# Kernel tuning notes

Hardware: AMD Instinct MI355X
Metric: run time of the kernel (lower is better)

## Reference

```python
import jax, jax.numpy as jnp
import numpy as np

N_HEADS = 16
ROPE_BASE = 10000.0


def _rotate_half(x):
    d = x.shape[-1] // 2
    return jnp.concatenate([-x[..., d:], x[..., :d]], axis=-1)


def _rope_tables(L, head_dim, dtype):
    inv_freq = 1.0 / (ROPE_BASE ** (jnp.arange(0, head_dim, 2, dtype=jnp.float32) / head_dim))
    t = jnp.arange(L, dtype=jnp.float32)
    freqs = jnp.outer(t, inv_freq)  # [L, head_dim//2]
    # torch code repeats cos/sin along last dim (tile x2) -> concat([c, c])
    cos = jnp.concatenate([jnp.cos(freqs), jnp.cos(freqs)], axis=-1).astype(dtype)
    sin = jnp.concatenate([jnp.sin(freqs), jnp.sin(freqs)], axis=-1).astype(dtype)
    return cos[None, None], sin[None, None]  # [1,1,L,head_dim]


def setup_inputs() -> dict:
    key = jax.random.key(0)
    kx, kq, kk, kv, ko = jax.random.split(key, 5)
    B, L, D = 4, 2048, 1024
    s = 0.02
    return {
        "x": jax.random.normal(kx, (B, L, D), dtype=jnp.float32),
        "Wq": jax.random.normal(kq, (D, D), dtype=jnp.float32) * s,
        "Wk": jax.random.normal(kk, (D, D), dtype=jnp.float32) * s,
        "Wv": jax.random.normal(kv, (D, D), dtype=jnp.float32) * s,
        "Wo": jax.random.normal(ko, (D, D), dtype=jnp.float32) * s,
    }


def reference(x, Wq, Wk, Wv, Wo):
    B, L, D = x.shape
    H = N_HEADS
    hd = D // H

    def split_heads(y):
        return y.reshape(B, L, H, hd).transpose(0, 2, 1, 3)  # [B,H,L,hd]

    q = split_heads(x @ Wq.T)
    k = split_heads(x @ Wk.T)
    v = split_heads(x @ Wv.T)

    cos, sin = _rope_tables(L, hd, x.dtype)
    q = q * cos + _rotate_half(q) * sin
    k = k * cos + _rotate_half(k) * sin

    scale = 1.0 / jnp.sqrt(jnp.asarray(hd, dtype=x.dtype))
    scores = jnp.einsum("bhqd,bhkd->bhqk", q, k) * scale
    attn = jax.nn.softmax(scores, axis=-1)
    out = jnp.einsum("bhqk,bhkd->bhqd", attn, v)
    out = out.transpose(0, 2, 1, 3).reshape(B, L, D)
    return out @ Wo.T
```

## Files before the change

kernel.cpp:

```cpp
#include <hip/hip_runtime.h>


typedef __bf16 bf16_t;
typedef __bf16 bf16x8 __attribute__((ext_vector_type(8)));
typedef __bf16 bf16x4 __attribute__((ext_vector_type(4)));
typedef float  floatx4 __attribute__((ext_vector_type(4)));
typedef unsigned int u32x2 __attribute__((ext_vector_type(2)));

#define B_  4
#define L_  2048
#define D_  1024
#define H_  16
#define HD_ 64
#define M_  (B_*L_)

__device__ __forceinline__ void async_copy16(const bf16_t* g, bf16_t* l) {
  __builtin_amdgcn_global_load_lds(
      (const __attribute__((address_space(1))) void*)g,
      (__attribute__((address_space(3))) void*)l, 16, 0, 0);
}

__device__ __forceinline__ unsigned int pack_bf16(float a, float b) {
  unsigned short ua = __builtin_bit_cast(unsigned short, (bf16_t)a);
  unsigned short ub = __builtin_bit_cast(unsigned short, (bf16_t)b);
  return (unsigned int)ua | ((unsigned int)ub << 16);
}

__global__ void prep_kernel(const float* __restrict__ x,
                            const float* __restrict__ wq, const float* __restrict__ wk,
                            const float* __restrict__ wv, const float* __restrict__ wo,
                            bf16_t* __restrict__ xb,
                            bf16_t* __restrict__ wqb, bf16_t* __restrict__ wkb,
                            bf16_t* __restrict__ wvb, bf16_t* __restrict__ wob,
                            float* __restrict__ cosT, float* __restrict__ sinT)
{
  const int NX = M_*D_;
  const int NW = D_*D_;
  int i = blockIdx.x*256 + threadIdx.x;
  if (i < NX) { xb[i] = (bf16_t)x[i]; return; }
  i -= NX;
  if (i < NW) { wqb[i] = (bf16_t)wq[i]; return; }
  i -= NW;
  if (i < NW) { wkb[i] = (bf16_t)wk[i]; return; }
  i -= NW;
  if (i < NW) { wvb[i] = (bf16_t)wv[i]; return; }
  i -= NW;
  if (i < NW) { wob[i] = (bf16_t)wo[i]; return; }
  i -= NW;
  if (i < L_*32) {
    int l = i >> 5, f = i & 31;
    double inv = pow(10000.0, -(double)f / 32.0);
    double ang = (double)l * inv;
    cosT[i] = (float)cos(ang);
    sinT[i] = (float)sin(ang);
  }
}

template<int MODE>
__global__ __launch_bounds__(256) void gemm_kernel(
    const bf16_t* __restrict__ A,
    const bf16_t* __restrict__ W0, const bf16_t* __restrict__ W1, const bf16_t* __restrict__ W2,
    bf16_t* __restrict__ C0, bf16_t* __restrict__ C1, bf16_t* __restrict__ C2,
    float* __restrict__ Cf,
    const float* __restrict__ cosT, const float* __restrict__ sinT)
{
  __shared__ __align__(16) bf16_t As[128*64];
  __shared__ __align__(16) bf16_t Bs[128*64];
  const int KD = 1024, ND = 1024;
  int z = (MODE==0) ? (int)blockIdx.z : 0;
  const bf16_t* W = (MODE==1) ? W0 : (z==0 ? W0 : (z==1 ? W1 : W2));
  int m0 = blockIdx.y*128, n0 = blockIdx.x*128;
  int tid = threadIdx.x;
  int wave = tid>>6, lane = tid&63, quad = lane>>4, lr = lane&15;
  int wm = wave>>1, wn = wave&1;
  int srow = lane>>3, sslot = lane&7;

  floatx4 zero4 = {0.f,0.f,0.f,0.f};
  floatx4 acc[4][4];
  #pragma unroll
  for (int i=0;i<4;i++)
    #pragma unroll
    for (int j=0;j<4;j++) acc[i][j] = zero4;

  #pragma unroll 1
  for (int k0 = 0; k0 < KD; k0 += 64) {
    #pragma unroll
    for (int j=0;j<4;j++) {
      int chunk = wave + j*4;
      int row = chunk*8 + srow;
      int col = ((sslot ^ (row&7)) << 3);
      async_copy16(A + (size_t)(m0+row)*KD + k0 + col, &As[chunk*512]);
      async_copy16(W + (size_t)(n0+row)*KD + k0 + col, &Bs[chunk*512]);
    }
    __syncthreads();
    #pragma unroll
    for (int ks=0; ks<2; ks++) {
      bf16x8 af[4], bfr[4];
      #pragma unroll
      for (int mi=0;mi<4;mi++)
        af[mi] = *(const bf16x8*)&As[(wm*64+mi*16+lr)*64 + (((ks*4+quad) ^ (lr&7))<<3)];
      #pragma unroll
      for (int ni=0;ni<4;ni++)
        bfr[ni] = *(const bf16x8*)&Bs[(wn*64+ni*16+lr)*64 + (((ks*4+quad) ^ (lr&7))<<3)];
      #pragma unroll
      for (int mi=0;mi<4;mi++)
        #pragma unroll
        for (int ni=0;ni<4;ni++)
          acc[mi][ni] = __builtin_amdgcn_mfma_f32_16x16x32_bf16(af[mi], bfr[ni], acc[mi][ni], 0,0,0);
    }
    __syncthreads();
  }

  if (MODE==1) {
    #pragma unroll
    for (int mi=0;mi<4;mi++) {
      int row = m0 + wm*64 + mi*16 + quad*4;
      #pragma unroll
      for (int ni=0;ni<4;ni++) {
        int col = n0 + wn*64 + ni*16 + lr;
        #pragma unroll
        for (int r=0;r<4;r++)
          Cf[(size_t)(row+r)*ND + col] = acc[mi][ni][r];
      }
    }
  } else if (z < 2) {
    bf16_t* Cb = (z==0) ? C0 : C1;
    const float sc = (z==0) ? 0.18033688011112042f : 1.0f;
    #pragma unroll
    for (int mi=0;mi<4;mi++) {
      int row = m0 + wm*64 + mi*16 + quad*4;
      int l = row & 2047;
      #pragma unroll
      for (int ni=0;ni<2;ni++) {
        int col = n0 + wn*64 + ni*16 + lr;
        int f = ni*16 + lr;
        #pragma unroll
        for (int r=0;r<4;r++) {
          float c = cosT[(l+r)*32 + f];
          float s = sinT[(l+r)*32 + f];
          float lo = acc[mi][ni][r], hi = acc[mi][ni+2][r];
          Cb[(size_t)(row+r)*ND + col]      = (bf16_t)((lo*c - hi*s)*sc);
          Cb[(size_t)(row+r)*ND + col + 32] = (bf16_t)((hi*c + lo*s)*sc);
        }
      }
    }
  } else {
    #pragma unroll
    for (int mi=0;mi<4;mi++) {
      int row0 = m0 + wm*64 + mi*16 + quad*4;
      int bb = row0 >> 11, ll = row0 & 2047;
      #pragma unroll
      for (int ni=0;ni<4;ni++) {
        int col = n0 + wn*64 + ni*16 + lr;
        int hh = col >> 6, dd = col & 63;
        uint2 val;
        val.x = pack_bf16(acc[mi][ni][0], acc[mi][ni][1]);
        val.y = pack_bf16(acc[mi][ni][2], acc[mi][ni][3]);
        *(uint2*)&C2[((size_t)((bb<<4)+hh)*64 + dd)*2048 + ll] = val;
      }
    }
  }
}

__global__ __launch_bounds__(256) void attn_kernel(
    const bf16_t* __restrict__ Q, const bf16_t* __restrict__ K,
    const bf16_t* __restrict__ Vt, bf16_t* __restrict__ Op,
    float* __restrict__ Ls)
{
  __shared__ __align__(16) bf16_t Ks[3][2048];
  __shared__ __align__(16) bf16_t Vs[3][2048];
  int tid = threadIdx.x;
  int wave = tid>>6, lane = tid&63, quad = lane>>4, lr = lane&15;
  int bh = blockIdx.x; int b = bh>>4, h = bh&15;
  int z = blockIdx.z;
  int q0 = blockIdx.y*128 + wave*32;
  size_t rowQ = (size_t)b*L_ + q0;
  int kvbase = z*1024;

  int slr = (lr&3) | ((lr&4)<<1) | ((lr&8)>>1);
  int vg  = ((lr>>2) ^ lr) & 3;

  int ksrow = wave*8 + (lane>>3);
  int kscol = (((lane&7) ^ (ksrow&7)) << 3);
  int vrow  = tid>>2;
  int vscol = (((lane&3) ^ (((vrow>>2)^vrow)&3)) << 3);

  bf16x8 qf[2][2];
  #pragma unroll
  for (int n=0;n<2;n++)
    #pragma unroll
    for (int ks=0;ks<2;ks++)
      qf[n][ks] = *(const bf16x8*)&Q[(rowQ + n*16 + lr)*D_ + h*HD_ + ks*32 + quad*8];

  const bf16_t* Kg = K + ((size_t)b*L_ + kvbase)*D_ + h*HD_;
  const bf16_t* Vg = Vt + ((size_t)bh*HD_)*L_ + kvbase;

  bf16x8 onesf;
  #pragma unroll
  for (int j=0;j<8;j++) onesf[j] = (bf16_t)1.0f;

  floatx4 zero4 = {0.f,0.f,0.f,0.f};
  floatx4 accO[2][4];
  floatx4 accS[2];
  accS[0] = zero4; accS[1] = zero4;
  #pragma unroll
  for (int n=0;n<2;n++)
    #pragma unroll
    for (int dt=0;dt<4;dt++) accO[n][dt] = zero4;

  auto stage = [&](int it, int c) {
    async_copy16(Kg + (size_t)(it*32 + ksrow)*D_ + kscol, &Ks[c][wave*512]);
    async_copy16(Vg + (size_t)vrow*L_ + it*32 + vscol,    &Vs[c][wave*512]);
  };

  stage(0, 0);
  stage(1, 1);
  asm volatile("s_waitcnt vmcnt(2)" ::: "memory");
  __builtin_amdgcn_s_barrier();

  #pragma unroll 1
  for (int it = 0; it < 32; ++it) {
    int c = it % 3;
    if (it < 30) stage(it+2, (it+2) % 3);

    floatx4 St[2][2];
    St[0][0]=zero4; St[0][1]=zero4; St[1][0]=zero4; St[1][1]=zero4;
    __builtin_amdgcn_s_setprio(1);
    #pragma unroll
    for (int t=0;t<2;t++) {
      #pragma unroll
      for (int ks=0;ks<2;ks++) {
        bf16x8 kf = *(const bf16x8*)&Ks[c][(t*16+slr)*64 + (((ks*4+quad) ^ (slr&7))<<3)];
        St[0][t] = __builtin_amdgcn_mfma_f32_16x16x32_bf16(kf, qf[0][ks], St[0][t], 0,0,0);
        St[1][t] = __builtin_amdgcn_mfma_f32_16x16x32_bf16(kf, qf[1][ks], St[1][t], 0,0,0);
      }
    }
    __builtin_amdgcn_s_setprio(0);

    bf16x8 pfv[2];
    #pragma unroll
    for (int n=0;n<2;n++) {
      unsigned int w00 = pack_bf16(exp2f(St[n][0][0]), exp2f(St[n][0][1]));
      unsigned int w01 = pack_bf16(exp2f(St[n][0][2]), exp2f(St[n][0][3]));
      unsigned int w10 = pack_bf16(exp2f(St[n][1][0]), exp2f(St[n][1][1]));
      unsigned int w11 = pack_bf16(exp2f(St[n][1][2]), exp2f(St[n][1][3]));
      u32x2 r0 = __builtin_amdgcn_permlane32_swap(w00, w10, false, false);
      u32x2 r1 = __builtin_amdgcn_permlane32_swap(w01, w11, false, false);
      union { unsigned int u[4]; bf16x8 v; } pu;
      pu.u[0] = r0.x; pu.u[1] = r1.x; pu.u[2] = r0.y; pu.u[3] = r1.y;
      pfv[n] = pu.v;
    }

    __builtin_amdgcn_s_setprio(1);
    #pragma unroll
    for (int dt=0;dt<4;dt++) {
      bf16x8 vf = *(const bf16x8*)&Vs[c][(dt*16+lr)*32 + ((quad ^ vg)<<3)];
      accO[0][dt] = __builtin_amdgcn_mfma_f32_16x16x32_bf16(vf, pfv[0], accO[0][dt], 0,0,0);
      accO[1][dt] = __builtin_amdgcn_mfma_f32_16x16x32_bf16(vf, pfv[1], accO[1][dt], 0,0,0);
    }
    accS[0] = __builtin_amdgcn_mfma_f32_16x16x32_bf16(onesf, pfv[0], accS[0], 0,0,0);
    accS[1] = __builtin_amdgcn_mfma_f32_16x16x32_bf16(onesf, pfv[1], accS[1], 0,0,0);
    __builtin_amdgcn_s_setprio(0);

    if (it < 30) {
      asm volatile("s_waitcnt vmcnt(2)" ::: "memory");
    } else {
      asm volatile("s_waitcnt vmcnt(0)" ::: "memory");
    }
    __builtin_amdgcn_s_barrier();
  }

  bf16_t* Opz = Op + (size_t)z*M_*D_;
  #pragma unroll
  for (int n=0;n<2;n++) {
    #pragma unroll
    for (int dt=0;dt<4;dt++) {
      uint2 w;
      w.x = pack_bf16(accO[n][dt][0], accO[n][dt][1]);
      w.y = pack_bf16(accO[n][dt][2], accO[n][dt][3]);
      *(uint2*)&Opz[(rowQ + n*16 + lr)*D_ + h*HD_ + dt*16 + quad*4] = w;
    }
  }
  if (quad == 0) {
    Ls[z*131072 + bh*2048 + q0 + lr]      = accS[0][0];
    Ls[z*131072 + bh*2048 + q0 + 16 + lr] = accS[1][0];
  }
}

__global__ void reduce_kernel(const bf16_t* __restrict__ Op, const float* __restrict__ Ls,
                              bf16_t* __restrict__ O)
{
  int i = blockIdx.x*256 + threadIdx.x;
  size_t e = (size_t)i*4;
  int d  = (int)(e & 1023);
  int bl = (int)(e >> 10);
  int bq = bl >> 11, l = bl & 2047, h = d >> 6;
  int li = (bq*16 + h)*2048 + l;
  float inv = 1.0f / (Ls[li] + Ls[li + 131072]);
  bf16x4 v0 = *(const bf16x4*)&Op[e];
  bf16x4 v1 = *(const bf16x4*)&Op[(size_t)M_*D_ + e];
  bf16x4 r;
  #pragma unroll
  for (int j=0;j<4;j++)
    r[j] = (bf16_t)(((float)v0[j] + (float)v1[j]) * inv);
  *(bf16x4*)&O[e] = r;
}

extern "C" void kernel_launch(void* const* d_in, const int* in_sizes, int n_in,
                              void* d_out, int out_size, void* d_ws, size_t ws_size,
                              hipStream_t stream) {
  const float* x  = (const float*)d_in[0];
  const float* wq = (const float*)d_in[1];
  const float* wk = (const float*)d_in[2];
  const float* wv = (const float*)d_in[3];
  const float* wo = (const float*)d_in[4];

  char* ws = (char*)d_ws;
  bf16_t* xb  = (bf16_t*)(ws);
  bf16_t* Qb  = (bf16_t*)(ws + (size_t)(16u<<20));
  bf16_t* Kb  = (bf16_t*)(ws + (size_t)(32u<<20));
  bf16_t* Vtb = (bf16_t*)(ws + (size_t)(48u<<20));
  bf16_t* wqb = (bf16_t*)(ws + (size_t)(64u<<20));
  bf16_t* wkb = (bf16_t*)(ws + (size_t)(66u<<20));
  bf16_t* wvb = (bf16_t*)(ws + (size_t)(68u<<20));
  bf16_t* wob = (bf16_t*)(ws + (size_t)(70u<<20));
  float* cosT = (float*)(ws + (size_t)(72u<<20));
  float* sinT = (float*)(ws + (size_t)(72u<<20) + (256u<<10));
  float* Ls   = (float*)wqb;
  bf16_t* Opart = (bf16_t*)d_out;
  bf16_t* Ob = xb;

  prep_kernel<<<49408, 256, 0, stream>>>(x, wq, wk, wv, wo, xb, wqb, wkb, wvb, wob, cosT, sinT);
  gemm_kernel<0><<<dim3(8,64,3), 256, 0, stream>>>(xb, wqb, wkb, wvb, Qb, Kb, Vtb, nullptr, cosT, sinT);
  attn_kernel<<<dim3(64,16,2), 256, 0, stream>>>(Qb, Kb, Vtb, Opart, Ls);
  reduce_kernel<<<8192, 256, 0, stream>>>(Opart, Ls, Ob);
  gemm_kernel<1><<<dim3(8,64,1), 256, 0, stream>>>(Ob, wob, nullptr, nullptr,
                                                   nullptr, nullptr, nullptr, (float*)d_out, cosT, sinT);
}
```

Measured before the change: 330.3 us.

## Drop split-KV attention and reduce kernel; use 64-key tiles with in-kernel normalization

Attention no longer splits the key range in two across blockIdx.z with a separate reduce kernel. Each block now walks the full key range with 64-key tiles in doubled LDS buffers and normalizes the output by the row sum before writing it. This removes the partial-output writes, the reduce launch and its memory traffic. In exchange there are half as many attention blocks (1024 instead of 2048) and more LDS per block, which can lower occupancy and latency hiding. The s_setprio hints are also dropped.

Result: no change. 326.2 us (-1.3%).

```diff
diff --git a/kernel.cpp b/kernel.cpp
--- a/kernel.cpp
+++ b/kernel.cpp
@@ -164,26 +164,20 @@
 
 __global__ __launch_bounds__(256) void attn_kernel(
     const bf16_t* __restrict__ Q, const bf16_t* __restrict__ K,
-    const bf16_t* __restrict__ Vt, bf16_t* __restrict__ Op,
-    float* __restrict__ Ls)
+    const bf16_t* __restrict__ Vt, bf16_t* __restrict__ O)
 {
-  __shared__ __align__(16) bf16_t Ks[3][2048];
-  __shared__ __align__(16) bf16_t Vs[3][2048];
+  __shared__ __align__(16) bf16_t Ks[3][4096];
+  __shared__ __align__(16) bf16_t Vs[3][4096];
   int tid = threadIdx.x;
   int wave = tid>>6, lane = tid&63, quad = lane>>4, lr = lane&15;
   int bh = blockIdx.x; int b = bh>>4, h = bh&15;
-  int z = blockIdx.z;
   int q0 = blockIdx.y*128 + wave*32;
   size_t rowQ = (size_t)b*L_ + q0;
-  int kvbase = z*1024;
 
   int slr = (lr&3) | ((lr&4)<<1) | ((lr&8)>>1);
-  int vg  = ((lr>>2) ^ lr) & 3;
-
-  int ksrow = wave*8 + (lane>>3);
-  int kscol = (((lane&7) ^ (ksrow&7)) << 3);
-  int vrow  = tid>>2;
-  int vscol = (((lane&3) ^ (((vrow>>2)^vrow)&3)) << 3);
+
+  int srow8 = lane>>3;
+  int sslot = lane&7;
 
   bf16x8 qf[2][2];
   #pragma unroll
@@ -192,8 +186,8 @@
     for (int ks=0;ks<2;ks++)
       qf[n][ks] = *(const bf16x8*)&Q[(rowQ + n*16 + lr)*D_ + h*HD_ + ks*32 + quad*8];
 
-  const bf16_t* Kg = K + ((size_t)b*L_ + kvbase)*D_ + h*HD_;
-  const bf16_t* Vg = Vt + ((size_t)bh*HD_)*L_ + kvbase;
+  const bf16_t* Kg = K + (size_t)b*L_*D_ + h*HD_;
+  const bf16_t* Vg = Vt + (size_t)bh*HD_*L_;
 
   bf16x8 onesf;
   #pragma unroll
@@ -209,13 +203,18 @@
     for (int dt=0;dt<4;dt++) accO[n][dt] = zero4;
 
   auto stage = [&](int it, int c) {
-    async_copy16(Kg + (size_t)(it*32 + ksrow)*D_ + kscol, &Ks[c][wave*512]);
-    async_copy16(Vg + (size_t)vrow*L_ + it*32 + vscol,    &Vs[c][wave*512]);
+    #pragma unroll
+    for (int j=0;j<2;j++) {
+      int row = wave*16 + j*8 + srow8;
+      int col = ((sslot ^ (row&7)) << 3);
+      async_copy16(Kg + (size_t)(it*64 + row)*D_ + col, &Ks[c][(wave*16 + j*8)*64]);
+      async_copy16(Vg + (size_t)row*L_ + it*64 + col,   &Vs[c][(wave*16 + j*8)*64]);
+    }
   };
 
   stage(0, 0);
   stage(1, 1);
-  asm volatile("s_waitcnt vmcnt(2)" ::: "memory");
+  asm volatile("s_waitcnt vmcnt(4)" ::: "memory");
   __builtin_amdgcn_s_barrier();
 
   #pragma unroll 1
@@ -223,11 +222,11 @@
     int c = it % 3;
     if (it < 30) stage(it+2, (it+2) % 3);
 
-    floatx4 St[2][2];
-    St[0][0]=zero4; St[0][1]=zero4; St[1][0]=zero4; St[1][1]=zero4;
-    __builtin_amdgcn_s_setprio(1);
-    #pragma unroll
-    for (int t=0;t<2;t++) {
+    floatx4 St[2][4];
+    #pragma unroll
+    for (int t=0;t<4;t++) { St[0][t]=zero4; St[1][t]=zero4; }
+    #pragma unroll
+    for (int t=0;t<4;t++) {
       #pragma unroll
       for (int ks=0;ks<2;ks++) {
         bf16x8 kf = *(const bf16x8*)&Ks[c][(t*16+slr)*64 + (((ks*4+quad) ^ (slr&7))<<3)];
@@ -235,75 +234,59 @@
         St[1][t] = __builtin_amdgcn_mfma_f32_16x16x32_bf16(kf, qf[1][ks], St[1][t], 0,0,0);
       }
     }
-    __builtin_amdgcn_s_setprio(0);
-
-    bf16x8 pfv[2];
+
+    bf16x8 pfv[2][2];
     #pragma unroll
     for (int n=0;n<2;n++) {
-      unsigned int w00 = pack_bf16(exp2f(St[n][0][0]), exp2f(St[n][0][1]));
-      unsigned int w01 = pack_bf16(exp2f(St[n][0][2]), exp2f(St[n][0][3]));
-      unsigned int w10 = pack_bf16(exp2f(St[n][1][0]), exp2f(St[n][1][1]));
-      unsigned int w11 = pack_bf16(exp2f(St[n][1][2]), exp2f(St[n][1][3]));
-      u32x2 r0 = __builtin_amdgcn_permlane32_swap(w00, w10, false, false);
-      u32x2 r1 = __builtin_amdgcn_permlane32_swap(w01, w11, false, false);
-      union { unsigned int u[4]; bf16x8 v; } pu;
-      pu.u[0] = r0.x; pu.u[1] = r1.x; pu.u[2] = r0.y; pu.u[3] = r1.y;
-      pfv[n] = pu.v;
-    }
-
-    __builtin_amdgcn_s_setprio(1);
+      #pragma unroll
+      for (int hh=0;hh<2;hh++) {
+        unsigned int w00 = pack_bf16(exp2f(St[n][2*hh][0]),   exp2f(St[n][2*hh][1]));
+        unsigned int w01 = pack_bf16(exp2f(St[n][2*hh][2]),   exp2f(St[n][2*hh][3]));
+        unsigned int w10 = pack_bf16(exp2f(St[n][2*hh+1][0]), exp2f(St[n][2*hh+1][1]));
+        unsigned int w11 = pack_bf16(exp2f(St[n][2*hh+1][2]), exp2f(St[n][2*hh+1][3]));
+        u32x2 r0 = __builtin_amdgcn_permlane32_swap(w00, w10, false, false);
+        u32x2 r1 = __builtin_amdgcn_permlane32_swap(w01, w11, false, false);
+        union { unsigned int u[4]; bf16x8 v; } pu;
+        pu.u[0] = r0.x; pu.u[1] = r1.x; pu.u[2] = r0.y; pu.u[3] = r1.y;
+        pfv[n][hh] = pu.v;
+      }
+    }
+
     #pragma unroll
     for (int dt=0;dt<4;dt++) {
-      bf16x8 vf = *(const bf16x8*)&Vs[c][(dt*16+lr)*32 + ((quad ^ vg)<<3)];
-      accO[0][dt] = __builtin_amdgcn_mfma_f32_16x16x32_bf16(vf, pfv[0], accO[0][dt], 0,0,0);
-      accO[1][dt] = __builtin_amdgcn_mfma_f32_16x16x32_bf16(vf, pfv[1], accO[1][dt], 0,0,0);
-    }
-    accS[0] = __builtin_amdgcn_mfma_f32_16x16x32_bf16(onesf, pfv[0], accS[0], 0,0,0);
-    accS[1] = __builtin_amdgcn_mfma_f32_16x16x32_bf16(onesf, pfv[1], accS[1], 0,0,0);
-    __builtin_amdgcn_s_setprio(0);
+      #pragma unroll
+      for (int hh=0;hh<2;hh++) {
+        bf16x8 vf = *(const bf16x8*)&Vs[c][(dt*16+lr)*64 + (((hh*4+quad) ^ (lr&7))<<3)];
+        accO[0][dt] = __builtin_amdgcn_mfma_f32_16x16x32_bf16(vf, pfv[0][hh], accO[0][dt], 0,0,0);
+        accO[1][dt] = __builtin_amdgcn_mfma_f32_16x16x32_bf16(vf, pfv[1][hh], accO[1][dt], 0,0,0);
+      }
+    }
+    accS[0] = __builtin_amdgcn_mfma_f32_16x16x32_bf16(onesf, pfv[0][0], accS[0], 0,0,0);
+    accS[1] = __builtin_amdgcn_mfma_f32_16x16x32_bf16(onesf, pfv[1][0], accS[1], 0,0,0);
+    accS[0] = __builtin_amdgcn_mfma_f32_16x16x32_bf16(onesf, pfv[0][1], accS[0], 0,0,0);
+    accS[1] = __builtin_amdgcn_mfma_f32_16x16x32_bf16(onesf, pfv[1][1], accS[1], 0,0,0);
 
     if (it < 30) {
-      asm volatile("s_waitcnt vmcnt(2)" ::: "memory");
+      asm volatile("s_waitcnt vmcnt(4)" ::: "memory");
     } else {
       asm volatile("s_waitcnt vmcnt(0)" ::: "memory");
     }
     __builtin_amdgcn_s_barrier();
   }
 
-  bf16_t* Opz = Op + (size_t)z*M_*D_;
+  float inv0 = 1.0f / accS[0][0];
+  float inv1 = 1.0f / accS[1][0];
   #pragma unroll
   for (int n=0;n<2;n++) {
+    float inv = n ? inv1 : inv0;
     #pragma unroll
     for (int dt=0;dt<4;dt++) {
       uint2 w;
-      w.x = pack_bf16(accO[n][dt][0], accO[n][dt][1]);
-      w.y = pack_bf16(accO[n][dt][2], accO[n][dt][3]);
-      *(uint2*)&Opz[(rowQ + n*16 + lr)*D_ + h*HD_ + dt*16 + quad*4] = w;
-    }
-  }
-  if (quad == 0) {
-    Ls[z*131072 + bh*2048 + q0 + lr]      = accS[0][0];
-    Ls[z*131072 + bh*2048 + q0 + 16 + lr] = accS[1][0];
-  }
-}
-
-__global__ void reduce_kernel(const bf16_t* __restrict__ Op, const float* __restrict__ Ls,
-                              bf16_t* __restrict__ O)
-{
-  int i = blockIdx.x*256 + threadIdx.x;
-  size_t e = (size_t)i*4;
-  int d  = (int)(e & 1023);
-  int bl = (int)(e >> 10);
-  int bq = bl >> 11, l = bl & 2047, h = d >> 6;
-  int li = (bq*16 + h)*2048 + l;
-  float inv = 1.0f / (Ls[li] + Ls[li + 131072]);
-  bf16x4 v0 = *(const bf16x4*)&Op[e];
-  bf16x4 v1 = *(const bf16x4*)&Op[(size_t)M_*D_ + e];
-  bf16x4 r;
-  #pragma unroll
-  for (int j=0;j<4;j++)
-    r[j] = (bf16_t)(((float)v0[j] + (float)v1[j]) * inv);
-  *(bf16x4*)&O[e] = r;
+      w.x = pack_bf16(accO[n][dt][0]*inv, accO[n][dt][1]*inv);
+      w.y = pack_bf16(accO[n][dt][2]*inv, accO[n][dt][3]*inv);
+      *(uint2*)&O[(rowQ + n*16 + lr)*D_ + h*HD_ + dt*16 + quad*4] = w;
+    }
+  }
 }
 
 extern "C" void kernel_launch(void* const* d_in, const int* in_sizes, int n_in,
@@ -326,14 +309,11 @@
   bf16_t* wob = (bf16_t*)(ws + (size_t)(70u<<20));
   float* cosT = (float*)(ws + (size_t)(72u<<20));
   float* sinT = (float*)(ws + (size_t)(72u<<20) + (256u<<10));
-  float* Ls   = (float*)wqb;
-  bf16_t* Opart = (bf16_t*)d_out;
   bf16_t* Ob = xb;
 
   prep_kernel<<<49408, 256, 0, stream>>>(x, wq, wk, wv, wo, xb, wqb, wkb, wvb, wob, cosT, sinT);
   gemm_kernel<0><<<dim3(8,64,3), 256, 0, stream>>>(xb, wqb, wkb, wvb, Qb, Kb, Vtb, nullptr, cosT, sinT);
-  attn_kernel<<<dim3(64,16,2), 256, 0, stream>>>(Qb, Kb, Vtb, Opart, Ls);
-  reduce_kernel<<<8192, 256, 0, stream>>>(Opart, Ls, Ob);
+  attn_kernel<<<dim3(64,16), 256, 0, stream>>>(Qb, Kb, Vtb, Ob);
   gemm_kernel<1><<<dim3(8,64,1), 256, 0, stream>>>(Ob, wob, nullptr, nullptr,
                                                    nullptr, nullptr, nullptr, (float*)d_out, cosT, sinT);
 }
```
